# Kernel optimization log

Measured on AMD Instinct MI355X. Metric: run time of the kernel, lower is better.

## Reference

```python
import jax, jax.numpy as jnp
import numpy as np

B, T, M, P = 256, 128, 64, 64


def setup_inputs() -> dict:
    key = jax.random.key(0)
    ks = jax.random.split(key, 20)
    s = 0.05
    inp = {
        "data": jax.random.normal(ks[0], (B, T - 1, 1), jnp.float32),
        "encoder_h": jax.random.normal(ks[1], (B, T, M), jnp.float32),
        "h0": jax.random.normal(ks[2], (B, P), jnp.float32),
        "s0": jax.random.normal(ks[3], (B, P), jnp.float32),
        # dense: Dense(1) on concat([x, context]) -> in=1+M
        "W_dense": jax.random.normal(ks[4], (1 + M, 1), jnp.float32) * s,
        "b_dense": jnp.zeros((1,), jnp.float32),
        # LSTM(p): kernel (1,4p), recurrent (p,4p), bias (4p); keras gate order i,f,c,o
        "Wk": jax.random.normal(ks[5], (1, 4 * P), jnp.float32) * s,
        "Uk": jax.random.normal(ks[6], (P, 4 * P), jnp.float32) * s,
        "bk": jnp.zeros((4 * P,), jnp.float32),
        # temporal attention: W_d Dense(m) on concat([h,c]) (2p -> m)
        "Wd": jax.random.normal(ks[7], (2 * P, M), jnp.float32) * s,
        "bWd": jnp.zeros((M,), jnp.float32),
        # U_d Dense(m) on encoder_h (m -> m)
        "Ud": jax.random.normal(ks[8], (M, M), jnp.float32) * s,
        "bUd": jnp.zeros((M,), jnp.float32),
        # v_d Dense(1)
        "vd": jax.random.normal(ks[9], (M, 1), jnp.float32) * s,
        "bvd": jnp.zeros((1,), jnp.float32),
        # dense_vb: Dense(1) on concat([h, context]) (p+m -> 1)
        "Wvb": jax.random.normal(ks[10], (P + M, 1), jnp.float32) * s,
        "bvb": jnp.zeros((1,), jnp.float32),
        # dense_Wb: Dense(p) applied AFTER dense_vb (1 -> p), as in the source
        "Wb": jax.random.normal(ks[11], (1, P), jnp.float32) * s,
        "bWb": jnp.zeros((P,), jnp.float32),
    }
    return inp


def reference(data, encoder_h, h0, s0, W_dense, b_dense, Wk, Uk, bk,
              Wd, bWd, Ud, bUd, vd, bvd, Wvb, bvb, Wb, bWb):
    # Loop-invariant: U_d(encoder_h), (B,T,M). Math identical to per-step compute.
    Ue = jnp.einsum('btm,mn->btn', encoder_h, Ud) + bUd

    def step(carry, x_t):
        ctx, _h = carry                      # ctx: (B,M)
        inp = jnp.concatenate([x_t, ctx], axis=-1)   # (B, 1+M)
        y = inp @ W_dense + b_dense                   # (B,1)
        # NOTE: source resets LSTM state to (h0, s0) at every step.
        z = y @ Wk + h0 @ Uk + bk                     # (B,4P)
        i_g, f_g, g_g, o_g = jnp.split(z, 4, axis=-1)
        c = jax.nn.sigmoid(f_g) * s0 + jax.nn.sigmoid(i_g) * jnp.tanh(g_g)
        h = jax.nn.sigmoid(o_g) * jnp.tanh(c)         # (B,P)
        # temporal attention
        dproj = jnp.concatenate([h, c], axis=-1) @ Wd + bWd   # (B,M)
        e = jnp.tanh(dproj[:, None, :] + Ue) @ vd + bvd        # (B,T,1)
        beta = jax.nn.softmax(e, axis=1)                       # (B,T,1)
        ctx_new = jnp.einsum('bti,btm->bm', beta, encoder_h)   # (B,M)
        return (ctx_new, h), None

    Bsz = encoder_h.shape[0]
    carry0 = (jnp.zeros((Bsz, Wk.shape[1] // 4 * 0 + encoder_h.shape[2]), encoder_h.dtype),
              jnp.zeros((Bsz, Uk.shape[0]), encoder_h.dtype))
    xs = jnp.transpose(data, (1, 0, 2))  # (T-1, B, 1)
    (ctx, h), _ = jax.lax.scan(step, carry0, xs)

    concatenated = jnp.concatenate([h, ctx], axis=-1)[:, None, :]  # (B,1,P+M)
    out = (concatenated @ Wvb + bvb) @ Wb + bWb                     # (B,1,P)
    return out
```

## Files before the change

### kernel.cpp

```cpp
#include <hip/hip_runtime.h>


#define Bn 256
#define Tn 128
#define Mn 64
#define Pn 64
#define NTH 512
#define NW 8
#define UST 68
#define DPST 72
#define HCST 132
#define K2C 2.885390081777927f

typedef float f32x2 __attribute__((ext_vector_type(2)));

__device__ __forceinline__ float fexp(float x) {
    return __builtin_amdgcn_exp2f(x * 1.44269504088896341f);
}
__device__ __forceinline__ float fexp2(float x) { return __builtin_amdgcn_exp2f(x); }
__device__ __forceinline__ float frcp(float x) { return __builtin_amdgcn_rcpf(x); }
__device__ __forceinline__ float fsig(float x) { return frcp(1.0f + fexp(-x)); }
__device__ __forceinline__ float ftanh(float x) { return 1.0f - 2.0f * frcp(1.0f + fexp(2.0f * x)); }

template <int CTRL>
__device__ __forceinline__ float dppmov(float x) {
    return __int_as_float(__builtin_amdgcn_update_dpp(
        0, __float_as_int(x), CTRL, 0xf, 0xf, false));
}
__device__ __forceinline__ float rdlane(float x, int l) {
    return __int_as_float(__builtin_amdgcn_readlane(__float_as_int(x), l));
}
__device__ __forceinline__ float wavesum63(float x) {
    x += dppmov<0x111>(x);
    x += dppmov<0x112>(x);
    x += dppmov<0x114>(x);
    x += dppmov<0x118>(x);
    x += dppmov<0x142>(x);
    x += dppmov<0x143>(x);
    return x;
}

#define OFF_ENC   0
#define OFF_UD    8704
#define OFF_PRE   13056
#define OFF_DPW   13312
#define OFF_HC    13888
#define OFF_YSDEN 14944
#define OFF_CTXP  14976
#define SMEM_FLOATS 15488

__global__ __launch_bounds__(NTH, 2)
void decoder_kernel(const float* __restrict__ data, const float* __restrict__ enc,
                    const float* __restrict__ h0, const float* __restrict__ s0,
                    const float* __restrict__ W_dense, const float* __restrict__ b_dense,
                    const float* __restrict__ Wk, const float* __restrict__ Uk,
                    const float* __restrict__ bk,
                    const float* __restrict__ Wd, const float* __restrict__ bWd,
                    const float* __restrict__ Ud, const float* __restrict__ bUd,
                    const float* __restrict__ vd, const float* __restrict__ bvd,
                    const float* __restrict__ Wvb, const float* __restrict__ bvb,
                    const float* __restrict__ Wb, const float* __restrict__ bWb,
                    float* __restrict__ out)
{
    extern __shared__ float smem[];
    float* enc_s  = smem + OFF_ENC;
    float* Ud_s   = smem + OFF_UD;
    float* pre_s  = smem + OFF_PRE;
    float* dprojw = smem + OFF_DPW;
    float* hcw    = smem + OFF_HC;
    f32x2* ysden  = (f32x2*)(smem + OFF_YSDEN);
    float* ctxp   = smem + OFF_CTXP;

    const int b    = blockIdx.x;
    const int tid  = threadIdx.x;
    const int lane = tid & 63;
    const int wv   = tid >> 6;

    {
        const float* encg = enc + (size_t)b * Tn * Mn;
        #pragma unroll
        for (int i = 0; i < 4; i++) {
            int flat = (i * NTH + tid) * 4;
            int t = flat >> 6, m = flat & 63;
            *(float4*)(enc_s + t * UST + m) = *(const float4*)(encg + flat);
        }
        #pragma unroll
        for (int i = 0; i < 2; i++) {
            int flat = (i * NTH + tid) * 4;
            int k = flat >> 6, n = flat & 63;
            *(float4*)(Ud_s + k * UST + n) = *(const float4*)(Ud + flat);
        }
        if (tid < 4 * Pn) {
            float s = bk[tid];
            const float* h0b = h0 + b * Pn;
            #pragma unroll
            for (int k = 0; k < Pn; k++) s = fmaf(h0b[k], Uk[k * 4 * Pn + tid], s);
            pre_s[tid] = s;
        }
        if (tid < 2 * NW) {
            f32x2 z; z.x = 0.0f; z.y = 0.125f;
            ysden[tid] = z;
        }
    }
    __syncthreads();

    const int t_e = 16 * wv + (lane >> 2), q_e = lane & 3, m0 = q_e * 16;
    f32x2 ue2[8];
    {
        float acc[16];
        #pragma unroll
        for (int j = 0; j < 16; j++) acc[j] = bUd[m0 + j];
        for (int k = 0; k < Mn; k++) {
            float a = enc_s[t_e * UST + k];
            const float4* ud = (const float4*)(Ud_s + k * UST + m0);
            #pragma unroll
            for (int j4 = 0; j4 < 4; j4++) {
                float4 u = ud[j4];
                acc[4 * j4 + 0] = fmaf(a, u.x, acc[4 * j4 + 0]);
                acc[4 * j4 + 1] = fmaf(a, u.y, acc[4 * j4 + 1]);
                acc[4 * j4 + 2] = fmaf(a, u.z, acc[4 * j4 + 2]);
                acc[4 * j4 + 3] = fmaf(a, u.w, acc[4 * j4 + 3]);
            }
        }
        #pragma unroll
        for (int j = 0; j < 8; j++) {
            ue2[j].x = K2C * acc[2 * j];
            ue2[j].y = K2C * acc[2 * j + 1];
        }
    }

    float enc_r[16];
    #pragma unroll
    for (int j = 0; j < 16; j++)
        enc_r[j] = enc_s[(16 * wv + j) * UST + lane];
    float wd_r[128];
    #pragma unroll
    for (int k = 0; k < 128; k++)
        wd_r[k] = K2C * Wd[k * Mn + lane];
    const float W0  = W_dense[0];
    const float bd  = b_dense[0];
    const float Wde = W_dense[1 + lane];
    const float wk_i = Wk[lane], wk_f = Wk[64 + lane],
                wk_g = Wk[128 + lane], wk_o = Wk[192 + lane];
    const float s0v   = s0[b * Pn + lane];
    const float bvd0  = bvd[0];
    const float bwd_l = K2C * bWd[lane];
    f32x2 vd2[8];
    float sumvd16 = 0.0f;
    #pragma unroll
    for (int j = 0; j < 8; j++) {
        float va = vd[m0 + 2 * j], vb = vd[m0 + 2 * j + 1];
        vd2[j].x = -2.0f * va; vd2[j].y = -2.0f * vb;
        sumvd16 += va + vb;
    }
    const float pre_i = pre_s[lane];
    const float pre_f = pre_s[64 + lane];
    const float pre_g = pre_s[128 + lane];
    const float pre_o = pre_s[192 + lane];
    const float* xb = data + (size_t)b * (Tn - 1);
    const float x_lo = xb[lane];
    const float x_hi = (lane < 63) ? xb[64 + lane] : 0.0f;

    float h = 0.0f, c = 0.0f;
    float* dp_my = dprojw + wv * DPST;
    float* hc_my = hcw + wv * HCST;

    for (int st = 0; st < Tn - 1; ++st) {
        const int par = st & 1, nxt = par ^ 1;

        f32x2 yv = ysden[par * NW + (lane & 7)];
        yv.x += dppmov<0x111>(yv.x); yv.y += dppmov<0x111>(yv.y);
        yv.x += dppmov<0x112>(yv.x); yv.y += dppmov<0x112>(yv.y);
        yv.x += dppmov<0x114>(yv.x); yv.y += dppmov<0x114>(yv.y);
        float ytot = rdlane(yv.x, 7);
        float dtot = rdlane(yv.y, 7);
        float xs = (st < 64) ? rdlane(x_lo, st) : rdlane(x_hi, st - 64);
        float y = fmaf(xs, W0, fmaf(ytot, frcp(dtot), bd));

        float zi = fmaf(y, wk_i, pre_i);
        float zf = fmaf(y, wk_f, pre_f);
        float zg = fmaf(y, wk_g, pre_g);
        float zo = fmaf(y, wk_o, pre_o);
        c = fsig(zf) * s0v + fsig(zi) * ftanh(zg);
        h = fsig(zo) * ftanh(c);

        {
            hc_my[lane] = h;
            hc_my[64 + lane] = c;
            float p0 = 0.0f, p1 = 0.0f, p2 = 0.0f, p3 = 0.0f;
            #pragma unroll
            for (int k4 = 0; k4 < 32; k4++) {
                float4 hv = *(const float4*)(hc_my + 4 * k4);
                p0 = fmaf(hv.x, wd_r[4 * k4 + 0], p0);
                p1 = fmaf(hv.y, wd_r[4 * k4 + 1], p1);
                p2 = fmaf(hv.z, wd_r[4 * k4 + 2], p2);
                p3 = fmaf(hv.w, wd_r[4 * k4 + 3], p3);
            }
            dp_my[lane] = ((p0 + p1) + (p2 + p3)) + bwd_l;
        }

        float ex;
        {
            float4 d[4];
            const float4* dp4 = (const float4*)(dp_my + m0);
            #pragma unroll
            for (int i = 0; i < 4; i++) d[i] = dp4[i];
            f32x2 accA; accA.x = sumvd16; accA.y = 0.0f;
            f32x2 accB; accB.x = 0.0f;    accB.y = 0.0f;
            #pragma unroll
            for (int i = 0; i < 4; i++) {
                f32x2 sA, rA, sB, rB;
                sA.x = d[i].x + ue2[2 * i].x;     sA.y = d[i].y + ue2[2 * i].y;
                rA.x = frcp(1.0f + fexp2(sA.x));  rA.y = frcp(1.0f + fexp2(sA.y));
                accA += vd2[2 * i] * rA;
                sB.x = d[i].z + ue2[2 * i + 1].x; sB.y = d[i].w + ue2[2 * i + 1].y;
                rB.x = frcp(1.0f + fexp2(sB.x));  rB.y = frcp(1.0f + fexp2(sB.y));
                accB += vd2[2 * i + 1] * rB;
            }
            f32x2 accT = accA + accB;
            float acc = accT.x + accT.y;
            acc += dppmov<0x111>(acc);
            acc += dppmov<0x112>(acc);
            ex = fexp(acc + bvd0);
        }

        {
            float p0 = 0.0f, p1 = 0.0f, p2 = 0.0f, p3 = 0.0f;
            #pragma unroll
            for (int j = 0; j < 4; j++) {
                p0 = fmaf(rdlane(ex, 4 * j + 3),        enc_r[j],      p0);
                p1 = fmaf(rdlane(ex, 4 * (j + 4) + 3),  enc_r[4 + j],  p1);
                p2 = fmaf(rdlane(ex, 4 * (j + 8) + 3),  enc_r[8 + j],  p2);
                p3 = fmaf(rdlane(ex, 4 * (j + 12) + 3), enc_r[12 + j], p3);
            }
            float ctxpart = (p0 + p1) + (p2 + p3);
            if (st == Tn - 2) ctxp[wv * 64 + lane] = ctxpart;
            f32x2 w2;
            w2.x = ctxpart * Wde;
            w2.y = ((lane & 3) == 3) ? ex : 0.0f;
            w2.x += dppmov<0x111>(w2.x); w2.y += dppmov<0x111>(w2.y);
            w2.x += dppmov<0x112>(w2.x); w2.y += dppmov<0x112>(w2.y);
            w2.x += dppmov<0x114>(w2.x); w2.y += dppmov<0x114>(w2.y);
            w2.x += dppmov<0x118>(w2.x); w2.y += dppmov<0x118>(w2.y);
            w2.x += dppmov<0x142>(w2.x); w2.y += dppmov<0x142>(w2.y);
            w2.x += dppmov<0x143>(w2.x); w2.y += dppmov<0x143>(w2.y);
            if (lane == 63) ysden[nxt * NW + wv] = w2;
        }
        __syncthreads();
    }

    if (wv == 0) {
        float dtot = 0.0f;
        #pragma unroll
        for (int w = 0; w < NW; w++) dtot += ysden[NW + w].y;
        float invS = frcp(dtot);
        float ctxm = 0.0f;
        #pragma unroll
        for (int w = 0; w < NW; w++) ctxm += ctxp[w * 64 + lane];
        ctxm *= invS;
        float part = h * Wvb[lane] + ctxm * Wvb[64 + lane];
        float v = rdlane(wavesum63(part), 63) + bvb[0];
        out[(size_t)b * Pn + lane] = fmaf(v, Wb[lane], bWb[lane]);
    }
}

extern "C" void kernel_launch(void* const* d_in, const int* in_sizes, int n_in,
                              void* d_out, int out_size, void* d_ws, size_t ws_size,
                              hipStream_t stream) {
    const float* data    = (const float*)d_in[0];
    const float* enc     = (const float*)d_in[1];
    const float* h0      = (const float*)d_in[2];
    const float* s0      = (const float*)d_in[3];
    const float* W_dense = (const float*)d_in[4];
    const float* b_dense = (const float*)d_in[5];
    const float* Wk      = (const float*)d_in[6];
    const float* Uk      = (const float*)d_in[7];
    const float* bk      = (const float*)d_in[8];
    const float* Wd      = (const float*)d_in[9];
    const float* bWd     = (const float*)d_in[10];
    const float* Ud      = (const float*)d_in[11];
    const float* bUd     = (const float*)d_in[12];
    const float* vd      = (const float*)d_in[13];
    const float* bvd     = (const float*)d_in[14];
    const float* Wvb     = (const float*)d_in[15];
    const float* bvb     = (const float*)d_in[16];
    const float* Wb      = (const float*)d_in[17];
    const float* bWb     = (const float*)d_in[18];

    decoder_kernel<<<Bn, NTH, SMEM_FLOATS * sizeof(float), stream>>>(
        data, enc, h0, s0, W_dense, b_dense, Wk, Uk, bk,
        Wd, bWd, Ud, bUd, vd, bvd, Wvb, bvb, Wb, bWb, (float*)d_out);
}
```

Baseline: 295.1 us.

## Split Wd projection across waves with readlane broadcast and LDS reduction

Each wave previously computed the full 128-term dproj dot product redundantly, keeping 128 Wd registers per lane and staging h/c through LDS. Now each wave handles a 16-row slice of [h,c], broadcasts the values with readlane, and writes a partial sum to LDS. After an added block barrier, the partials are summed. This cuts per-wave FMAs and register pressure, at the cost of an extra __syncthreads per recurrent step and a cross-wave LDS reduction.

After: 283.7 us. 1.04x faster.

```diff
diff --git a/kernel.cpp b/kernel.cpp
--- a/kernel.cpp
+++ b/kernel.cpp
@@ -9,7 +9,6 @@
 #define NW 8
 #define UST 68
 #define DPST 72
-#define HCST 132
 #define K2C 2.885390081777927f
 
 typedef float f32x2 __attribute__((ext_vector_type(2)));
@@ -43,11 +42,11 @@
 #define OFF_ENC   0
 #define OFF_UD    8704
 #define OFF_PRE   13056
-#define OFF_DPW   13312
-#define OFF_HC    13888
-#define OFF_YSDEN 14944
-#define OFF_CTXP  14976
-#define SMEM_FLOATS 15488
+#define OFF_DPART 13312
+#define OFF_DPW   13888
+#define OFF_YSDEN 14464
+#define OFF_CTXP  14496
+#define SMEM_FLOATS 15008
 
 __global__ __launch_bounds__(NTH, 2)
 void decoder_kernel(const float* __restrict__ data, const float* __restrict__ enc,
@@ -66,8 +65,8 @@
     float* enc_s  = smem + OFF_ENC;
     float* Ud_s   = smem + OFF_UD;
     float* pre_s  = smem + OFF_PRE;
+    float* dpart  = smem + OFF_DPART;
     float* dprojw = smem + OFF_DPW;
-    float* hcw    = smem + OFF_HC;
     f32x2* ysden  = (f32x2*)(smem + OFF_YSDEN);
     float* ctxp   = smem + OFF_CTXP;
 
@@ -133,10 +132,10 @@
     #pragma unroll
     for (int j = 0; j < 16; j++)
         enc_r[j] = enc_s[(16 * wv + j) * UST + lane];
-    float wd_r[128];
+    float wd_r[16];
     #pragma unroll
-    for (int k = 0; k < 128; k++)
-        wd_r[k] = K2C * Wd[k * Mn + lane];
+    for (int j = 0; j < 16; j++)
+        wd_r[j] = K2C * Wd[(16 * wv + j) * Mn + lane];
     const float W0  = W_dense[0];
     const float bd  = b_dense[0];
     const float Wde = W_dense[1 + lane];
@@ -157,13 +156,14 @@
     const float pre_f = pre_s[64 + lane];
     const float pre_g = pre_s[128 + lane];
     const float pre_o = pre_s[192 + lane];
+    const bool hv_sel = (wv < 4);
+    const int  base16 = (wv & 3) * 16;
     const float* xb = data + (size_t)b * (Tn - 1);
     const float x_lo = xb[lane];
     const float x_hi = (lane < 63) ? xb[64 + lane] : 0.0f;
 
     float h = 0.0f, c = 0.0f;
     float* dp_my = dprojw + wv * DPST;
-    float* hc_my = hcw + wv * HCST;
 
     for (int st = 0; st < Tn - 1; ++st) {
         const int par = st & 1, nxt = par ^ 1;
@@ -185,18 +185,25 @@
         h = fsig(zo) * ftanh(c);
 
         {
-            hc_my[lane] = h;
-            hc_my[64 + lane] = c;
+            float hv = hv_sel ? h : c;
             float p0 = 0.0f, p1 = 0.0f, p2 = 0.0f, p3 = 0.0f;
             #pragma unroll
-            for (int k4 = 0; k4 < 32; k4++) {
-                float4 hv = *(const float4*)(hc_my + 4 * k4);
-                p0 = fmaf(hv.x, wd_r[4 * k4 + 0], p0);
-                p1 = fmaf(hv.y, wd_r[4 * k4 + 1], p1);
-                p2 = fmaf(hv.z, wd_r[4 * k4 + 2], p2);
-                p3 = fmaf(hv.w, wd_r[4 * k4 + 3], p3);
+            for (int j = 0; j < 4; j++) {
+                p0 = fmaf(rdlane(hv, base16 + j),      wd_r[j],      p0);
+                p1 = fmaf(rdlane(hv, base16 + 4 + j),  wd_r[4 + j],  p1);
+                p2 = fmaf(rdlane(hv, base16 + 8 + j),  wd_r[8 + j],  p2);
+                p3 = fmaf(rdlane(hv, base16 + 12 + j), wd_r[12 + j], p3);
             }
-            dp_my[lane] = ((p0 + p1) + (p2 + p3)) + bwd_l;
+            dpart[wv * DPST + lane] = (p0 + p1) + (p2 + p3);
+        }
+        __syncthreads();
+
+        {
+            float v0 = dpart[0 * DPST + lane] + dpart[1 * DPST + lane];
+            float v1 = dpart[2 * DPST + lane] + dpart[3 * DPST + lane];
+            float v2 = dpart[4 * DPST + lane] + dpart[5 * DPST + lane];
+            float v3 = dpart[6 * DPST + lane] + dpart[7 * DPST + lane];
+            dp_my[lane] = ((v0 + v1) + (v2 + v3)) + bwd_l;
         }
 
         float ex;
```
